# Kernel optimization log

Measured on AMD Instinct MI355X. Metric: run time of the kernel, lower is better.

## Reference

```python
import jax, jax.numpy as jnp
import numpy as np
import math

NUM_HEADS = 16
CONSTITUENCY_PENALTY = 0.5
CONSTITUENT_BLOCK = 64  # deterministic stand-in for the ChomskyParser constituency spans


def constituency_penalty_mask(seq_len, dtype):
    # Tokens in the same constituent (contiguous block) attend freely;
    # cross-constituent pairs are penalized by CONSTITUENCY_PENALTY.
    blk = jnp.arange(seq_len) // CONSTITUENT_BLOCK
    return jnp.where(blk[:, None] != blk[None, :], CONSTITUENCY_PENALTY, 0.0).astype(dtype)


def setup_inputs() -> dict:
    key = jax.random.key(0)
    ks = jax.random.split(key, 7)
    B, S, H = 8, 1024, 1024
    scale = 1.0 / math.sqrt(H)
    return {
        "hidden_states": jax.random.normal(ks[0], (B, S, H), jnp.float32),
        "Wq": jax.random.normal(ks[1], (H, H), jnp.float32) * scale,
        "bq": jnp.zeros((H,), jnp.float32),
        "Wk": jax.random.normal(ks[2], (H, H), jnp.float32) * scale,
        "bk": jnp.zeros((H,), jnp.float32),
        "Wv": jax.random.normal(ks[3], (H, H), jnp.float32) * scale,
        "bv": jnp.zeros((H,), jnp.float32),
    }


def reference(hidden_states, Wq, bq, Wk, bk, Wv, bv):
    B, S, H = hidden_states.shape
    nh = NUM_HEADS
    hd = H // nh

    def heads(x):  # [B,S,H] -> [B,nh,S,hd]
        return x.reshape(B, S, nh, hd).transpose(0, 2, 1, 3)

    q = heads(hidden_states @ Wq + bq)
    k = heads(hidden_states @ Wk + bk)
    v = heads(hidden_states @ Wv + bv)

    scores = jnp.einsum("bhqd,bhkd->bhqk", q, k) / jnp.sqrt(jnp.asarray(hd, q.dtype))
    # constituency penalty subtracted before softmax (broadcast over batch, heads)
    scores = scores - constituency_penalty_mask(S, scores.dtype)[None, None, :, :]
    probs = jax.nn.softmax(scores, axis=-1)  # dropout is identity in eval

    ctx = jnp.einsum("bhqk,bhkd->bhqd", probs, v)
    ctx = ctx.transpose(0, 2, 1, 3).reshape(B, S, H)
    return ctx
```

## Files before the change

### kernel.cpp

```cpp
#include <hip/hip_runtime.h>
#include <cstdint>

#define BB 8
#define SQ 1024
#define HH 1024
#define NH 16
#define HD 64

typedef __attribute__((ext_vector_type(4))) float f32x4;
typedef __attribute__((ext_vector_type(8))) __bf16 bf16x8;
typedef __attribute__((ext_vector_type(8))) unsigned short u16x8;
typedef __attribute__((ext_vector_type(4))) unsigned short u16x4;

__device__ __forceinline__ unsigned short f2bf(float f){
  uint32_t u = __builtin_bit_cast(uint32_t, f);
  u += 0x7FFFu + ((u >> 16) & 1u);
  return (unsigned short)(u >> 16);
}

__device__ __forceinline__ void gload_lds16(const void* g, void* l){
  __builtin_amdgcn_global_load_lds((__attribute__((address_space(1))) void*)g,
                                   (__attribute__((address_space(3))) void*)l,
                                   16, 0, 0);
}

__global__ __launch_bounds__(256) void k_convert_x(const float* __restrict__ x,
                                                   unsigned short* __restrict__ xb){
  int i = blockIdx.x * 256 + threadIdx.x;
  const f32x4* xv = (const f32x4*)x;
  f32x4 a = xv[2*i], b = xv[2*i+1];
  u16x8 o;
  o[0]=f2bf(a[0]); o[1]=f2bf(a[1]); o[2]=f2bf(a[2]); o[3]=f2bf(a[3]);
  o[4]=f2bf(b[0]); o[5]=f2bf(b[1]); o[6]=f2bf(b[2]); o[7]=f2bf(b[3]);
  ((u16x8*)xb)[i] = o;
}

__global__ __launch_bounds__(256) void k_wt(const float* __restrict__ Wq,
                                            const float* __restrict__ Wk,
                                            const float* __restrict__ Wv,
                                            unsigned short* __restrict__ wt){
  __shared__ float t[32][33];
  int p = blockIdx.z;
  const float* W = (p==0)?Wq:((p==1)?Wk:Wv);
  int n0 = blockIdx.x*32, k0 = blockIdx.y*32;
  int tx = threadIdx.x, ty = threadIdx.y;
  #pragma unroll
  for(int j=0;j<32;j+=8) t[ty+j][tx] = W[(size_t)(k0+ty+j)*HH + n0+tx];
  __syncthreads();
  unsigned short* o = wt + (size_t)p*HH*HH;
  #pragma unroll
  for(int j=0;j<32;j+=8) o[(size_t)(n0+ty+j)*HH + k0+tx] = f2bf(t[tx][ty+j]);
}

#define BM 128
#define BN 128
#define BK 64
__global__ __launch_bounds__(256) void k_qkv(const unsigned short* __restrict__ Xb,
                                             const unsigned short* __restrict__ Wt,
                                             const float* __restrict__ bq,
                                             const float* __restrict__ bk,
                                             const float* __restrict__ bv,
                                             unsigned short* __restrict__ q_ws,
                                             unsigned short* __restrict__ k_ws,
                                             unsigned short* __restrict__ vt_ws){
  __shared__ __align__(16) unsigned short As[2][BM*BK];
  __shared__ __align__(16) unsigned short Bs[2][BN*BK];
  int tid = threadIdx.x;
  int lane = tid & 63, wid = tid >> 6;
  int bid = blockIdx.x;
  int sw = (bid & 7)*192 + (bid >> 3);
  int nt = sw % 24, mt = sw / 24;
  int m0 = mt*BM, n0 = nt*BN;
  int wm = (wid & 1)*64, wn = (wid >> 1)*64;
  int lr = lane & 15, g = lane >> 4;

  int srow = tid >> 3;
  int sch  = (tid & 7) ^ (srow & 7);

  const f32x4 zf = {0.f,0.f,0.f,0.f};
  f32x4 acc[4][4];
  #pragma unroll
  for(int a=0;a<4;a++)
    #pragma unroll
    for(int b=0;b<4;b++) acc[a][b] = zf;

  #pragma unroll
  for(int it=0; it<4; it++){
    int row = it*32 + srow, slot = it*256 + tid;
    gload_lds16(Xb + (size_t)(m0+row)*1024 + sch*8, &As[0][slot*8]);
    gload_lds16(Wt + (size_t)(n0+row)*1024 + sch*8, &Bs[0][slot*8]);
  }
  __syncthreads();

  int cur = 0;
  for(int kk=0; kk<16; kk++){
    if(kk < 15){
      int kb = (kk+1)*BK;
      #pragma unroll
      for(int it=0; it<4; it++){
        int row = it*32 + srow, slot = it*256 + tid;
        gload_lds16(Xb + (size_t)(m0+row)*1024 + kb + sch*8, &As[cur^1][slot*8]);
        gload_lds16(Wt + (size_t)(n0+row)*1024 + kb + sch*8, &Bs[cur^1][slot*8]);
      }
    }
    #pragma unroll
    for(int ks=0; ks<2; ks++){
      bf16x8 af[4], bfr[4];
      #pragma unroll
      for(int mi=0;mi<4;mi++){
        int r = wm + mi*16 + lr;
        af[mi] = *(const bf16x8*)&As[cur][r*64 + (((ks*4+g) ^ (r&7))<<3)];
      }
      #pragma unroll
      for(int ni=0;ni<4;ni++){
        int r = wn + ni*16 + lr;
        bfr[ni] = *(const bf16x8*)&Bs[cur][r*64 + (((ks*4+g) ^ (r&7))<<3)];
      }
      #pragma unroll
      for(int mi=0;mi<4;mi++)
        #pragma unroll
        for(int ni=0;ni<4;ni++)
          acc[mi][ni] = __builtin_amdgcn_mfma_f32_16x16x32_bf16(af[mi], bfr[ni], acc[mi][ni], 0,0,0);
    }
    __syncthreads();
    cur ^= 1;
  }

  int proj = n0 >> 10;
  const float* bias = (proj==0)?bq:((proj==1)?bk:bv);
  const float QSCALE = 0.18033688f;
  #pragma unroll
  for(int mi=0;mi<4;mi++){
    #pragma unroll
    for(int ni=0;ni<4;ni++){
      int ncol = n0 + wn + ni*16 + lr;
      int hcol = ncol & 1023;
      int h = hcol >> 6, d = hcol & 63;
      float bval = bias[hcol];
      if(proj == 0){
        #pragma unroll
        for(int i=0;i<4;i++){
          int m = m0 + wm + mi*16 + g*4 + i;
          int b = m >> 10, s = m & 1023;
          q_ws[((size_t)(b*NH + h)*SQ + s)*HD + d] = f2bf((acc[mi][ni][i] + bval)*QSCALE);
        }
      } else if(proj == 1){
        #pragma unroll
        for(int i=0;i<4;i++){
          int m = m0 + wm + mi*16 + g*4 + i;
          int b = m >> 10, s = m & 1023;
          k_ws[((size_t)(b*NH + h)*SQ + s)*HD + d] = f2bf(acc[mi][ni][i] + bval);
        }
      } else {
        int m = m0 + wm + mi*16 + g*4;
        int b = m >> 10, s = m & 1023;
        u16x4 pk;
        #pragma unroll
        for(int i=0;i<4;i++) pk[i] = f2bf(acc[mi][ni][i] + bval);
        *(u16x4*)&vt_ws[((size_t)(b*NH + h)*HD + d)*SQ + s] = pk;
      }
    }
  }
}

__global__ __launch_bounds__(256) void k_attn(const unsigned short* __restrict__ q_ws,
                                              const unsigned short* __restrict__ k_ws,
                                              const unsigned short* __restrict__ vt_ws,
                                              float* __restrict__ out){
  __shared__ __align__(16) unsigned short Ks[2][64*64];
  __shared__ __align__(16) unsigned short Vs[2][64*64];
  __shared__ __align__(16) unsigned short Ps[4][32*64];
  int tid = threadIdx.x, lane = tid & 63, wid = tid >> 6;
  int lr = lane & 15, g = lane >> 4;
  int bid = blockIdx.x;
  int swz = (bid & 7)*128 + (bid >> 3);
  int qb = swz & 7, bh = swz >> 3;
  int qw = qb*128 + wid*32;
  const unsigned short* qp = q_ws + (size_t)bh*SQ*HD;
  const unsigned short* kp = k_ws + (size_t)bh*SQ*HD;
  const unsigned short* vp = vt_ws + (size_t)bh*HD*SQ;

  bf16x8 qf[2][2];
  #pragma unroll
  for(int ns=0;ns<2;ns++)
    #pragma unroll
    for(int ks=0;ks<2;ks++)
      qf[ns][ks] = *(const bf16x8*)&qp[(size_t)(qw + ns*16 + lr)*HD + ks*32 + g*8];

  int diag = qw >> 6;

  int srow = tid >> 3;
  int sch  = (tid & 7) ^ (srow & 7);

  const f32x4 zf = {0.f,0.f,0.f,0.f};
  float lacc[2] = {0.f, 0.f};
  f32x4 co[4][2];
  #pragma unroll
  for(int ms=0;ms<4;ms++)
    #pragma unroll
    for(int ns=0;ns<2;ns++) co[ms][ns] = zf;

  unsigned short* Pw = &Ps[wid][0];

  #pragma unroll
  for(int it=0; it<2; it++){
    int row = it*32 + srow, slot = it*256 + tid;
    gload_lds16(kp + (size_t)row*HD + sch*8, &Ks[0][slot*8]);
    gload_lds16(vp + (size_t)row*SQ + sch*8, &Vs[0][slot*8]);
  }
  __syncthreads();

  int cur = 0;
  for(int kt=0; kt<16; kt++){
    if(kt < 15){
      int kb = (kt+1)*64;
      #pragma unroll
      for(int it=0; it<2; it++){
        int row = it*32 + srow, slot = it*256 + tid;
        gload_lds16(kp + (size_t)(kb+row)*HD + sch*8, &Ks[cur^1][slot*8]);
        gload_lds16(vp + (size_t)row*SQ + kb + sch*8, &Vs[cur^1][slot*8]);
      }
    }

    f32x4 sc[4][2];
    #pragma unroll
    for(int ms=0;ms<4;ms++){
      int r = ms*16 + lr;
      bf16x8 kf0 = *(const bf16x8*)&Ks[cur][r*64 + ((g ^ (r&7))<<3)];
      bf16x8 kf1 = *(const bf16x8*)&Ks[cur][r*64 + (((4+g) ^ (r&7))<<3)];
      #pragma unroll
      for(int ns=0;ns<2;ns++){
        sc[ms][ns] = __builtin_amdgcn_mfma_f32_16x16x32_bf16(kf0, qf[ns][0], zf, 0,0,0);
        sc[ms][ns] = __builtin_amdgcn_mfma_f32_16x16x32_bf16(kf1, qf[ns][1], sc[ms][ns], 0,0,0);
      }
    }

    float add = (kt == diag) ? 0.72134752f : 0.0f;

    #pragma unroll
    for(int ms=0;ms<4;ms++){
      #pragma unroll
      for(int ns=0;ns<2;ns++){
        u16x4 pk;
        #pragma unroll
        for(int i=0;i<4;i++){
          float pv = __builtin_amdgcn_exp2f(sc[ms][ns][i] + add);
          lacc[ns] += pv;
          pk[i] = f2bf(pv);
        }
        int q = ns*16 + lr;
        int c = ms*2 + (g>>1);
        *(u16x4*)&Pw[q*64 + ((c ^ (q&7))<<3) + (g&1)*4] = pk;
      }
    }

    #pragma unroll
    for(int ms=0;ms<4;ms++){
      int vr = ms*16 + lr;
      bf16x8 vf0 = *(const bf16x8*)&Vs[cur][vr*64 + ((g ^ (vr&7))<<3)];
      bf16x8 vf1 = *(const bf16x8*)&Vs[cur][vr*64 + (((4+g) ^ (vr&7))<<3)];
      #pragma unroll
      for(int ns=0;ns<2;ns++){
        int q = ns*16 + lr;
        bf16x8 pf0 = *(const bf16x8*)&Pw[q*64 + ((g ^ (q&7))<<3)];
        bf16x8 pf1 = *(const bf16x8*)&Pw[q*64 + (((4+g) ^ (q&7))<<3)];
        co[ms][ns] = __builtin_amdgcn_mfma_f32_16x16x32_bf16(vf0, pf0, co[ms][ns], 0,0,0);
        co[ms][ns] = __builtin_amdgcn_mfma_f32_16x16x32_bf16(vf1, pf1, co[ms][ns], 0,0,0);
      }
    }

    __syncthreads();
    cur ^= 1;
  }

  float rl[2];
  #pragma unroll
  for(int ns=0;ns<2;ns++){
    float l = lacc[ns];
    l += __shfl_xor(l, 16);
    l += __shfl_xor(l, 32);
    rl[ns] = 1.0f / l;
  }
  int b = bh >> 4, h = bh & 15;
  #pragma unroll
  for(int ms=0;ms<4;ms++){
    #pragma unroll
    for(int ns=0;ns<2;ns++){
      int q = qw + ns*16 + lr;
      int d = h*HD + ms*16 + g*4;
      f32x4 r = co[ms][ns];
      r[0]*=rl[ns]; r[1]*=rl[ns]; r[2]*=rl[ns]; r[3]*=rl[ns];
      *(f32x4*)&out[((size_t)(b*SQ + q))*HH + d] = r;
    }
  }
}

extern "C" void kernel_launch(void* const* d_in, const int* in_sizes, int n_in,
                              void* d_out, int out_size, void* d_ws, size_t ws_size,
                              hipStream_t stream){
  const float* hs = (const float*)d_in[0];
  const float* Wq = (const float*)d_in[1];
  const float* bq = (const float*)d_in[2];
  const float* Wk = (const float*)d_in[3];
  const float* bk = (const float*)d_in[4];
  const float* Wv = (const float*)d_in[5];
  const float* bv = (const float*)d_in[6];
  float* out = (float*)d_out;

  unsigned char* ws = (unsigned char*)d_ws;
  const size_t NX = (size_t)8192*1024;
  unsigned short* xb    = (unsigned short*)ws;
  unsigned short* wt    = (unsigned short*)(ws + NX*2);
  unsigned short* q_ws  = (unsigned short*)(ws + NX*2 + (size_t)3*1024*1024*2);
  unsigned short* k_ws  = q_ws + NX;
  unsigned short* vt_ws = k_ws + NX;

  k_convert_x<<<4096, 256, 0, stream>>>(hs, xb);
  k_wt<<<dim3(32,32,3), dim3(32,8), 0, stream>>>(Wq, Wk, Wv, wt);
  k_qkv<<<24*64, 256, 0, stream>>>(xb, wt, bq, bk, bv, q_ws, k_ws, vt_ws);
  k_attn<<<1024, 256, 0, stream>>>(q_ws, k_ws, vt_ws, out);
}
```

Baseline: 226.4 us.

## Restructure QKV GEMM to 256x128 tiles with 8 waves and triple-buffered prefetch

The QKV projection GEMM now uses 256x128 block tiles with 512 threads (8 waves in a 2x4 layout) and a three-stage LDS ring. Global-to-LDS prefetch for tile k+2 is split into pieces interleaved between MFMA phases, and each phase is bracketed by s_setprio and raw s_barrier with explicit vmcnt waits. The aim is to hide global load latency and raise MFMA utilisation through more reuse per tile. In exchange LDS use grows to about 144KB per block, which limits occupancy to one block per CU, and the hand-placed waitcnt and barrier logic is fragile.

```diff
diff --git a/kernel.cpp b/kernel.cpp
--- a/kernel.cpp
+++ b/kernel.cpp
@@ -52,10 +52,10 @@
   for(int j=0;j<32;j+=8) o[(size_t)(n0+ty+j)*HH + k0+tx] = f2bf(t[tx][ty+j]);
 }
 
-#define BM 128
-#define BN 128
-#define BK 64
-__global__ __launch_bounds__(256) void k_qkv(const unsigned short* __restrict__ Xb,
+#define QBM 256
+#define QBN 128
+#define QBK 64
+__global__ __launch_bounds__(512) void k_qkv(const unsigned short* __restrict__ Xb,
                                              const unsigned short* __restrict__ Wt,
                                              const float* __restrict__ bq,
                                              const float* __restrict__ bk,
@@ -63,96 +63,151 @@
                                              unsigned short* __restrict__ q_ws,
                                              unsigned short* __restrict__ k_ws,
                                              unsigned short* __restrict__ vt_ws){
-  __shared__ __align__(16) unsigned short As[2][BM*BK];
-  __shared__ __align__(16) unsigned short Bs[2][BN*BK];
+  __shared__ __align__(16) unsigned short As[3][QBM*QBK];
+  __shared__ __align__(16) unsigned short Bs[3][QBN*QBK];
   int tid = threadIdx.x;
   int lane = tid & 63, wid = tid >> 6;
+  int wr = wid >> 2, wc = wid & 3;
   int bid = blockIdx.x;
-  int sw = (bid & 7)*192 + (bid >> 3);
+  int sw = (bid & 7)*96 + (bid >> 3);
   int nt = sw % 24, mt = sw / 24;
-  int m0 = mt*BM, n0 = nt*BN;
-  int wm = (wid & 1)*64, wn = (wid >> 1)*64;
+  int m0 = mt*QBM, n0 = nt*QBN;
   int lr = lane & 15, g = lane >> 4;
 
   int srow = tid >> 3;
   int sch  = (tid & 7) ^ (srow & 7);
 
   const f32x4 zf = {0.f,0.f,0.f,0.f};
-  f32x4 acc[4][4];
-  #pragma unroll
-  for(int a=0;a<4;a++)
-    #pragma unroll
-    for(int b=0;b<4;b++) acc[a][b] = zf;
-
-  #pragma unroll
-  for(int it=0; it<4; it++){
-    int row = it*32 + srow, slot = it*256 + tid;
-    gload_lds16(Xb + (size_t)(m0+row)*1024 + sch*8, &As[0][slot*8]);
-    gload_lds16(Wt + (size_t)(n0+row)*1024 + sch*8, &Bs[0][slot*8]);
-  }
-  __syncthreads();
+  f32x4 acc[8][2];
+  #pragma unroll
+  for(int a=0;a<8;a++){ acc[a][0] = zf; acc[a][1] = zf; }
+
+  #define STAGE_A(buf, kb, it) do{ \
+    int row_ = (it)*64 + srow; int slot_ = (it)*512 + tid; \
+    gload_lds16(Xb + (size_t)(m0+row_)*1024 + (kb) + sch*8, &As[buf][slot_*8]); }while(0)
+  #define STAGE_B(buf, kb, it) do{ \
+    int row_ = (it)*64 + srow; int slot_ = (it)*512 + tid; \
+    gload_lds16(Wt + (size_t)(n0+row_)*1024 + (kb) + sch*8, &Bs[buf][slot_*8]); }while(0)
+
+  STAGE_A(0,0,0); STAGE_A(0,0,1); STAGE_A(0,0,2); STAGE_A(0,0,3);
+  STAGE_B(0,0,0); STAGE_B(0,0,1);
+  STAGE_A(1,QBK,0); STAGE_A(1,QBK,1); STAGE_A(1,QBK,2); STAGE_A(1,QBK,3);
+  STAGE_B(1,QBK,0); STAGE_B(1,QBK,1);
+  asm volatile("s_waitcnt vmcnt(6)" ::: "memory");
+  __builtin_amdgcn_s_barrier();
 
   int cur = 0;
-  for(int kk=0; kk<16; kk++){
-    if(kk < 15){
-      int kb = (kk+1)*BK;
-      #pragma unroll
-      for(int it=0; it<4; it++){
-        int row = it*32 + srow, slot = it*256 + tid;
-        gload_lds16(Xb + (size_t)(m0+row)*1024 + kb + sch*8, &As[cur^1][slot*8]);
-        gload_lds16(Wt + (size_t)(n0+row)*1024 + kb + sch*8, &Bs[cur^1][slot*8]);
-      }
-    }
-    #pragma unroll
-    for(int ks=0; ks<2; ks++){
-      bf16x8 af[4], bfr[4];
-      #pragma unroll
-      for(int mi=0;mi<4;mi++){
-        int r = wm + mi*16 + lr;
-        af[mi] = *(const bf16x8*)&As[cur][r*64 + (((ks*4+g) ^ (r&7))<<3)];
-      }
-      #pragma unroll
-      for(int ni=0;ni<4;ni++){
-        int r = wn + ni*16 + lr;
-        bfr[ni] = *(const bf16x8*)&Bs[cur][r*64 + (((ks*4+g) ^ (r&7))<<3)];
-      }
-      #pragma unroll
-      for(int mi=0;mi<4;mi++)
-        #pragma unroll
-        for(int ni=0;ni<4;ni++)
-          acc[mi][ni] = __builtin_amdgcn_mfma_f32_16x16x32_bf16(af[mi], bfr[ni], acc[mi][ni], 0,0,0);
-    }
-    __syncthreads();
-    cur ^= 1;
-  }
+  for(int kt=0; kt<16; kt++){
+    const unsigned short* Ab = As[cur];
+    const unsigned short* Bb = Bs[cur];
+    int nb = cur+2; if(nb>=3) nb-=3;
+    bool pf = (kt < 14);
+    int kb2 = (kt+2)*QBK;
+
+    bf16x8 bfr[2], af[4];
+    #pragma unroll
+    for(int ni=0;ni<2;ni++){
+      int r = wc*32 + ni*16 + lr;
+      bfr[ni] = *(const bf16x8*)&Bb[r*64 + ((g ^ (r&7))<<3)];
+    }
+    #pragma unroll
+    for(int mi=0;mi<4;mi++){
+      int r = wr*128 + mi*16 + lr;
+      af[mi] = *(const bf16x8*)&Ab[r*64 + ((g ^ (r&7))<<3)];
+    }
+    if(pf){ STAGE_A(nb,kb2,0); STAGE_A(nb,kb2,1); }
+    __builtin_amdgcn_s_setprio(1);
+    #pragma unroll
+    for(int mi=0;mi<4;mi++)
+      #pragma unroll
+      for(int ni=0;ni<2;ni++)
+        acc[mi][ni] = __builtin_amdgcn_mfma_f32_16x16x32_bf16(af[mi], bfr[ni], acc[mi][ni], 0,0,0);
+    __builtin_amdgcn_s_setprio(0);
+    __builtin_amdgcn_s_barrier();
+
+    #pragma unroll
+    for(int mi=0;mi<4;mi++){
+      int r = wr*128 + (mi+4)*16 + lr;
+      af[mi] = *(const bf16x8*)&Ab[r*64 + ((g ^ (r&7))<<3)];
+    }
+    if(pf){ STAGE_A(nb,kb2,2); STAGE_A(nb,kb2,3); }
+    __builtin_amdgcn_s_setprio(1);
+    #pragma unroll
+    for(int mi=0;mi<4;mi++)
+      #pragma unroll
+      for(int ni=0;ni<2;ni++)
+        acc[mi+4][ni] = __builtin_amdgcn_mfma_f32_16x16x32_bf16(af[mi], bfr[ni], acc[mi+4][ni], 0,0,0);
+    __builtin_amdgcn_s_setprio(0);
+    __builtin_amdgcn_s_barrier();
+
+    #pragma unroll
+    for(int ni=0;ni<2;ni++){
+      int r = wc*32 + ni*16 + lr;
+      bfr[ni] = *(const bf16x8*)&Bb[r*64 + (((4+g) ^ (r&7))<<3)];
+    }
+    #pragma unroll
+    for(int mi=0;mi<4;mi++){
+      int r = wr*128 + mi*16 + lr;
+      af[mi] = *(const bf16x8*)&Ab[r*64 + (((4+g) ^ (r&7))<<3)];
+    }
+    if(pf){ STAGE_B(nb,kb2,0); STAGE_B(nb,kb2,1); }
+    __builtin_amdgcn_s_setprio(1);
+    #pragma unroll
+    for(int mi=0;mi<4;mi++)
+      #pragma unroll
+      for(int ni=0;ni<2;ni++)
+        acc[mi][ni] = __builtin_amdgcn_mfma_f32_16x16x32_bf16(af[mi], bfr[ni], acc[mi][ni], 0,0,0);
+    __builtin_amdgcn_s_setprio(0);
+    __builtin_amdgcn_s_barrier();
+
+    #pragma unroll
+    for(int mi=0;mi<4;mi++){
+      int r = wr*128 + (mi+4)*16 + lr;
+      af[mi] = *(const bf16x8*)&Ab[r*64 + (((4+g) ^ (r&7))<<3)];
+    }
+    __builtin_amdgcn_s_setprio(1);
+    #pragma unroll
+    for(int mi=0;mi<4;mi++)
+      #pragma unroll
+      for(int ni=0;ni<2;ni++)
+        acc[mi+4][ni] = __builtin_amdgcn_mfma_f32_16x16x32_bf16(af[mi], bfr[ni], acc[mi+4][ni], 0,0,0);
+    __builtin_amdgcn_s_setprio(0);
+
+    if(kt < 14)       asm volatile("s_waitcnt vmcnt(6)" ::: "memory");
+    else if(kt == 14) asm volatile("s_waitcnt vmcnt(0)" ::: "memory");
+    __builtin_amdgcn_s_barrier();
+    cur++; if(cur>=3) cur-=3;
+  }
+  #undef STAGE_A
+  #undef STAGE_B
 
   int proj = n0 >> 10;
   const float* bias = (proj==0)?bq:((proj==1)?bk:bv);
   const float QSCALE = 0.18033688f;
   #pragma unroll
-  for(int mi=0;mi<4;mi++){
-    #pragma unroll
-    for(int ni=0;ni<4;ni++){
-      int ncol = n0 + wn + ni*16 + lr;
+  for(int mi=0;mi<8;mi++){
+    #pragma unroll
+    for(int ni=0;ni<2;ni++){
+      int ncol = n0 + wc*32 + ni*16 + lr;
       int hcol = ncol & 1023;
       int h = hcol >> 6, d = hcol & 63;
       float bval = bias[hcol];
       if(proj == 0){
         #pragma unroll
         for(int i=0;i<4;i++){
-          int m = m0 + wm + mi*16 + g*4 + i;
+          int m = m0 + wr*128 + mi*16 + g*4 + i;
           int b = m >> 10, s = m & 1023;
           q_ws[((size_t)(b*NH + h)*SQ + s)*HD + d] = f2bf((acc[mi][ni][i] + bval)*QSCALE);
         }
       } else if(proj == 1){
         #pragma unroll
         for(int i=0;i<4;i++){
-          int m = m0 + wm + mi*16 + g*4 + i;
+          int m = m0 + wr*128 + mi*16 + g*4 + i;
           int b = m >> 10, s = m & 1023;
           k_ws[((size_t)(b*NH + h)*SQ + s)*HD + d] = f2bf(acc[mi][ni][i] + bval);
         }
       } else {
-        int m = m0 + wm + mi*16 + g*4;
+        int m = m0 + wr*128 + mi*16 + g*4;
         int b = m >> 10, s = m & 1023;
         u16x4 pk;
         #pragma unroll
@@ -317,6 +372,6 @@
 
   k_convert_x<<<4096, 256, 0, stream>>>(hs, xb);
   k_wt<<<dim3(32,32,3), dim3(32,8), 0, stream>>>(Wq, Wk, Wv, wt);
-  k_qkv<<<24*64, 256, 0, stream>>>(xb, wt, bq, bk, bv, q_ws, k_ws, vt_ws);
+  k_qkv<<<768, 512, 0, stream>>>(xb, wt, bq, bk, bv, q_ws, k_ws, vt_ws);
   k_attn<<<1024, 256, 0, stream>>>(q_ws, k_ws, vt_ws, out);
 }
```

Result: slower. 236.3 us (+4.4%).
